# Performance work log

Measured on AMD Instinct MI355X. Metric: run time of the kernel, lower is better.

## Reference

```python
import jax, jax.numpy as jnp
import numpy as np

TWO_PI = 2.0 * np.pi
PI = np.pi
RESONANCE_WEIGHT = 0.1


def setup_inputs() -> dict:
    key = jax.random.key(0)
    k1, k2, k3, k4, k5 = jax.random.split(key, 5)
    B, C = 16384, 1000          # batch, num classes for the CE term
    N, E = 4096, 131072         # graph nodes, directed edges (avg degree 32)
    outputs = jax.random.normal(k1, (B, C), dtype=jnp.float32)
    targets = jax.random.randint(k2, (B,), 0, C)
    resonance_phase = jax.random.normal(k3, (N, N), dtype=jnp.float32)
    edge_src = jax.random.randint(k4, (E,), 0, N)
    edge_dst = jax.random.randint(k5, (E,), 0, N)
    return {"outputs": outputs, "targets": targets,
            "resonance_phase": resonance_phase,
            "edge_src": edge_src, "edge_dst": edge_dst}


def reference(outputs, targets, resonance_phase, edge_src, edge_dst):
    # base_criterion: CrossEntropyLoss (mean reduction over batch)
    logp = jax.nn.log_softmax(outputs, axis=-1)                      # [B, C]
    base_loss = -jnp.mean(jnp.take_along_axis(logp, targets[:, None], axis=1))

    # resonance term: vectorized gather over all topology edges
    phase_ij = resonance_phase[edge_src, edge_dst]                   # [E]
    phase_ji = resonance_phase[edge_dst, edge_src]                   # [E]
    d = jnp.abs(phase_ij - phase_ji) % TWO_PI
    d = jnp.where(d > PI, TWO_PI - d, d)                             # wrap to [0, pi]
    resonance_loss = jnp.sum(d) / d.shape[0]                         # / total_connections

    return base_loss + RESONANCE_WEIGHT * resonance_loss
```

## Files before the change

kernel.cpp:

```cpp
#include <hip/hip_runtime.h>
#include <math.h>

#define TWO_PI_F 6.28318530717958647692f
#define PI_F     3.14159265358979323846f

__global__ __launch_bounds__(256) void fused_kernel(
    const float* __restrict__ outputs,
    const int*   __restrict__ targets,
    const float* __restrict__ phase,
    const int*   __restrict__ esrc,
    const int*   __restrict__ edst,
    int B, int C, int N, int E,
    int res_blocks,
    float invB, float scaleE,
    float* __restrict__ ws)
{
    __shared__ float part[4];
    const int lane = threadIdx.x & 63;
    const int wave = threadIdx.x >> 6;

    float wsum = 0.0f;

    if ((int)blockIdx.x < res_blocks) {
        const int i = blockIdx.x * blockDim.x + threadIdx.x;
        float d = 0.0f;
        if (i < E) {
            const int s = esrc[i];
            const int t = edst[i];
            const float a = phase[(size_t)s * (size_t)N + (size_t)t];
            const float b = phase[(size_t)t * (size_t)N + (size_t)s];
            d = fabsf(a - b);
            d = fmodf(d, TWO_PI_F);
            if (d > PI_F) d = TWO_PI_F - d;
        }
        #pragma unroll
        for (int off = 32; off; off >>= 1)
            d += __shfl_xor(d, off, 64);
        if (lane == 0) wsum = d * scaleE;
    } else {
        const int row = (blockIdx.x - res_blocks) * 4 + wave;
        if (row < B) {
            const float*  rowp = outputs + (size_t)row * (size_t)C;
            const float4* row4 = (const float4*)rowp;
            const int nf4 = C >> 2;

            float m, s;
            if (nf4 <= 256) {
                const float4 NEG = make_float4(-INFINITY, -INFINITY, -INFINITY, -INFINITY);
                const int j0 = lane, j1 = lane + 64, j2 = lane + 128, j3 = lane + 192;
                float4 v0 = (j0 < nf4) ? row4[j0] : NEG;
                float4 v1 = (j1 < nf4) ? row4[j1] : NEG;
                float4 v2 = (j2 < nf4) ? row4[j2] : NEG;
                float4 v3 = (j3 < nf4) ? row4[j3] : NEG;
                const int remBase = nf4 << 2;
                const bool hasTail = (remBase + lane) < C;
                float tail = hasTail ? rowp[remBase + lane] : -INFINITY;

                m = tail;
                m = fmaxf(m, fmaxf(fmaxf(v0.x, v0.y), fmaxf(v0.z, v0.w)));
                m = fmaxf(m, fmaxf(fmaxf(v1.x, v1.y), fmaxf(v1.z, v1.w)));
                m = fmaxf(m, fmaxf(fmaxf(v2.x, v2.y), fmaxf(v2.z, v2.w)));
                m = fmaxf(m, fmaxf(fmaxf(v3.x, v3.y), fmaxf(v3.z, v3.w)));
                #pragma unroll
                for (int off = 32; off; off >>= 1)
                    m = fmaxf(m, __shfl_xor(m, off, 64));

                s  = __expf(v0.x - m) + __expf(v0.y - m) + __expf(v0.z - m) + __expf(v0.w - m);
                s += __expf(v1.x - m) + __expf(v1.y - m) + __expf(v1.z - m) + __expf(v1.w - m);
                s += __expf(v2.x - m) + __expf(v2.y - m) + __expf(v2.z - m) + __expf(v2.w - m);
                s += __expf(v3.x - m) + __expf(v3.y - m) + __expf(v3.z - m) + __expf(v3.w - m);
                s += __expf(tail - m);
                #pragma unroll
                for (int off = 32; off; off >>= 1)
                    s += __shfl_xor(s, off, 64);
            } else {
                m = -INFINITY;
                for (int j = lane; j < nf4; j += 64) {
                    float4 x = row4[j];
                    m = fmaxf(m, fmaxf(fmaxf(x.x, x.y), fmaxf(x.z, x.w)));
                }
                const int remBase = nf4 << 2;
                if (remBase + lane < C) m = fmaxf(m, rowp[remBase + lane]);
                #pragma unroll
                for (int off = 32; off; off >>= 1)
                    m = fmaxf(m, __shfl_xor(m, off, 64));

                s = 0.0f;
                for (int j = lane; j < nf4; j += 64) {
                    float4 x = row4[j];
                    s += __expf(x.x - m) + __expf(x.y - m)
                       + __expf(x.z - m) + __expf(x.w - m);
                }
                if (remBase + lane < C) s += __expf(rowp[remBase + lane] - m);
                #pragma unroll
                for (int off = 32; off; off >>= 1)
                    s += __shfl_xor(s, off, 64);
            }

            if (lane == 0) {
                const int t = targets[row];
                const float tv = rowp[t];
                wsum = (m + __logf(s) - tv) * invB;
            }
        }
    }

    if (lane == 0) part[wave] = wsum;
    __syncthreads();
    if (threadIdx.x == 0)
        ws[blockIdx.x] = part[0] + part[1] + part[2] + part[3];
}

__global__ __launch_bounds__(256) void reduce_kernel(
    const float* __restrict__ ws, int P, float* __restrict__ out)
{
    float s = 0.0f;
    for (int i = threadIdx.x; i < P; i += 256)
        s += ws[i];
    #pragma unroll
    for (int off = 32; off; off >>= 1)
        s += __shfl_xor(s, off, 64);

    __shared__ float part[4];
    if ((threadIdx.x & 63) == 0) part[threadIdx.x >> 6] = s;
    __syncthreads();
    if (threadIdx.x == 0)
        out[0] = part[0] + part[1] + part[2] + part[3];
}

extern "C" void kernel_launch(void* const* d_in, const int* in_sizes, int n_in,
                              void* d_out, int out_size, void* d_ws, size_t ws_size,
                              hipStream_t stream) {
    const float* outputs = (const float*)d_in[0];
    const int*   targets = (const int*)d_in[1];
    const float* phase   = (const float*)d_in[2];
    const int*   esrc    = (const int*)d_in[3];
    const int*   edst    = (const int*)d_in[4];

    const int B = in_sizes[1];
    const int C = in_sizes[0] / B;
    const int E = in_sizes[3];
    int N = 1;
    while ((long long)N * (long long)N < (long long)in_sizes[2]) N++;

    const int res_blocks = (E + 255) / 256;
    const int ce_blocks  = (B + 3) / 4;
    const int grid = res_blocks + ce_blocks;

    float* ws = (float*)d_ws;

    fused_kernel<<<grid, 256, 0, stream>>>(outputs, targets, phase, esrc, edst,
                                           B, C, N, E, res_blocks,
                                           1.0f / (float)B, 0.1f / (float)E,
                                           ws);
    reduce_kernel<<<1, 256, 0, stream>>>(ws, grid, (float*)d_out);
}
```

Baseline: 148.4 us.

## Process four edges per thread and two CE rows per wave

The resonance branch now has each thread load four edges through int4 index loads and issue eight independent phase gathers, which cuts the resonance block count by four. The cross-entropy branch has each wave handle two rows in sequence, halving the CE block count, and the target value load is moved earlier. The aim is to raise memory-level parallelism per thread and reduce block launch and partial-sum overhead, at the cost of more registers and fewer total waves to hide latency. Helper functions factor out the warp reductions and the shared per-row CE code.

Result: no change. 149.7 us (+0.9%).

```diff
diff --git a/kernel.cpp b/kernel.cpp
--- a/kernel.cpp
+++ b/kernel.cpp
@@ -3,6 +3,72 @@
 
 #define TWO_PI_F 6.28318530717958647692f
 #define PI_F     3.14159265358979323846f
+
+__device__ __forceinline__ float warp_sum(float s) {
+    #pragma unroll
+    for (int off = 32; off; off >>= 1) s += __shfl_xor(s, off, 64);
+    return s;
+}
+__device__ __forceinline__ float warp_max(float m) {
+    #pragma unroll
+    for (int off = 32; off; off >>= 1) m = fmaxf(m, __shfl_xor(m, off, 64));
+    return m;
+}
+
+__device__ __forceinline__ float edge_wrap(float a, float b) {
+    float d = fabsf(a - b);
+    d = fmodf(d, TWO_PI_F);
+    return (d > PI_F) ? (TWO_PI_F - d) : d;
+}
+
+__device__ __forceinline__ float ce_row(const float* __restrict__ rowp,
+                                        int C, int lane, int t) {
+    const float4* row4 = (const float4*)rowp;
+    const int nf4 = C >> 2;
+    const float tv = rowp[t];
+    float m, s;
+    if (nf4 <= 256) {
+        const float4 NEG = make_float4(-INFINITY, -INFINITY, -INFINITY, -INFINITY);
+        const int j0 = lane, j1 = lane + 64, j2 = lane + 128, j3 = lane + 192;
+        float4 v0 = (j0 < nf4) ? row4[j0] : NEG;
+        float4 v1 = (j1 < nf4) ? row4[j1] : NEG;
+        float4 v2 = (j2 < nf4) ? row4[j2] : NEG;
+        float4 v3 = (j3 < nf4) ? row4[j3] : NEG;
+        const int remBase = nf4 << 2;
+        float tail = (remBase + lane < C) ? rowp[remBase + lane] : -INFINITY;
+
+        m = tail;
+        m = fmaxf(m, fmaxf(fmaxf(v0.x, v0.y), fmaxf(v0.z, v0.w)));
+        m = fmaxf(m, fmaxf(fmaxf(v1.x, v1.y), fmaxf(v1.z, v1.w)));
+        m = fmaxf(m, fmaxf(fmaxf(v2.x, v2.y), fmaxf(v2.z, v2.w)));
+        m = fmaxf(m, fmaxf(fmaxf(v3.x, v3.y), fmaxf(v3.z, v3.w)));
+        m = warp_max(m);
+
+        s  = __expf(v0.x - m) + __expf(v0.y - m) + __expf(v0.z - m) + __expf(v0.w - m);
+        s += __expf(v1.x - m) + __expf(v1.y - m) + __expf(v1.z - m) + __expf(v1.w - m);
+        s += __expf(v2.x - m) + __expf(v2.y - m) + __expf(v2.z - m) + __expf(v2.w - m);
+        s += __expf(v3.x - m) + __expf(v3.y - m) + __expf(v3.z - m) + __expf(v3.w - m);
+        s += __expf(tail - m);
+        s = warp_sum(s);
+    } else {
+        m = -INFINITY;
+        for (int j = lane; j < nf4; j += 64) {
+            float4 x = row4[j];
+            m = fmaxf(m, fmaxf(fmaxf(x.x, x.y), fmaxf(x.z, x.w)));
+        }
+        const int remBase = nf4 << 2;
+        if (remBase + lane < C) m = fmaxf(m, rowp[remBase + lane]);
+        m = warp_max(m);
+        s = 0.0f;
+        for (int j = lane; j < nf4; j += 64) {
+            float4 x = row4[j];
+            s += __expf(x.x - m) + __expf(x.y - m) + __expf(x.z - m) + __expf(x.w - m);
+        }
+        if (remBase + lane < C) s += __expf(rowp[remBase + lane] - m);
+        s = warp_sum(s);
+    }
+    return m + __logf(s) - tv;
+}
 
 __global__ __launch_bounds__(256) void fused_kernel(
     const float* __restrict__ outputs,
@@ -22,86 +88,41 @@
     float wsum = 0.0f;
 
     if ((int)blockIdx.x < res_blocks) {
-        const int i = blockIdx.x * blockDim.x + threadIdx.x;
+        const int base = (blockIdx.x * 256 + threadIdx.x) * 4;
         float d = 0.0f;
-        if (i < E) {
-            const int s = esrc[i];
-            const int t = edst[i];
-            const float a = phase[(size_t)s * (size_t)N + (size_t)t];
-            const float b = phase[(size_t)t * (size_t)N + (size_t)s];
-            d = fabsf(a - b);
-            d = fmodf(d, TWO_PI_F);
-            if (d > PI_F) d = TWO_PI_F - d;
+        if (base + 3 < E) {
+            const int4 s4 = *(const int4*)(esrc + base);
+            const int4 t4 = *(const int4*)(edst + base);
+            const float a0 = phase[(size_t)s4.x * (size_t)N + (size_t)t4.x];
+            const float b0 = phase[(size_t)t4.x * (size_t)N + (size_t)s4.x];
+            const float a1 = phase[(size_t)s4.y * (size_t)N + (size_t)t4.y];
+            const float b1 = phase[(size_t)t4.y * (size_t)N + (size_t)s4.y];
+            const float a2 = phase[(size_t)s4.z * (size_t)N + (size_t)t4.z];
+            const float b2 = phase[(size_t)t4.z * (size_t)N + (size_t)s4.z];
+            const float a3 = phase[(size_t)s4.w * (size_t)N + (size_t)t4.w];
+            const float b3 = phase[(size_t)t4.w * (size_t)N + (size_t)s4.w];
+            d = edge_wrap(a0, b0) + edge_wrap(a1, b1)
+              + edge_wrap(a2, b2) + edge_wrap(a3, b3);
+        } else {
+            for (int i = base; i < E; i++) {
+                const int s = esrc[i], t = edst[i];
+                d += edge_wrap(phase[(size_t)s * (size_t)N + (size_t)t],
+                               phase[(size_t)t * (size_t)N + (size_t)s]);
+            }
         }
-        #pragma unroll
-        for (int off = 32; off; off >>= 1)
-            d += __shfl_xor(d, off, 64);
+        d = warp_sum(d);
         if (lane == 0) wsum = d * scaleE;
     } else {
-        const int row = (blockIdx.x - res_blocks) * 4 + wave;
-        if (row < B) {
-            const float*  rowp = outputs + (size_t)row * (size_t)C;
-            const float4* row4 = (const float4*)rowp;
-            const int nf4 = C >> 2;
-
-            float m, s;
-            if (nf4 <= 256) {
-                const float4 NEG = make_float4(-INFINITY, -INFINITY, -INFINITY, -INFINITY);
-                const int j0 = lane, j1 = lane + 64, j2 = lane + 128, j3 = lane + 192;
-                float4 v0 = (j0 < nf4) ? row4[j0] : NEG;
-                float4 v1 = (j1 < nf4) ? row4[j1] : NEG;
-                float4 v2 = (j2 < nf4) ? row4[j2] : NEG;
-                float4 v3 = (j3 < nf4) ? row4[j3] : NEG;
-                const int remBase = nf4 << 2;
-                const bool hasTail = (remBase + lane) < C;
-                float tail = hasTail ? rowp[remBase + lane] : -INFINITY;
-
-                m = tail;
-                m = fmaxf(m, fmaxf(fmaxf(v0.x, v0.y), fmaxf(v0.z, v0.w)));
-                m = fmaxf(m, fmaxf(fmaxf(v1.x, v1.y), fmaxf(v1.z, v1.w)));
-                m = fmaxf(m, fmaxf(fmaxf(v2.x, v2.y), fmaxf(v2.z, v2.w)));
-                m = fmaxf(m, fmaxf(fmaxf(v3.x, v3.y), fmaxf(v3.z, v3.w)));
-                #pragma unroll
-                for (int off = 32; off; off >>= 1)
-                    m = fmaxf(m, __shfl_xor(m, off, 64));
-
-                s  = __expf(v0.x - m) + __expf(v0.y - m) + __expf(v0.z - m) + __expf(v0.w - m);
-                s += __expf(v1.x - m) + __expf(v1.y - m) + __expf(v1.z - m) + __expf(v1.w - m);
-                s += __expf(v2.x - m) + __expf(v2.y - m) + __expf(v2.z - m) + __expf(v2.w - m);
-                s += __expf(v3.x - m) + __expf(v3.y - m) + __expf(v3.z - m) + __expf(v3.w - m);
-                s += __expf(tail - m);
-                #pragma unroll
-                for (int off = 32; off; off >>= 1)
-                    s += __shfl_xor(s, off, 64);
-            } else {
-                m = -INFINITY;
-                for (int j = lane; j < nf4; j += 64) {
-                    float4 x = row4[j];
-                    m = fmaxf(m, fmaxf(fmaxf(x.x, x.y), fmaxf(x.z, x.w)));
-                }
-                const int remBase = nf4 << 2;
-                if (remBase + lane < C) m = fmaxf(m, rowp[remBase + lane]);
-                #pragma unroll
-                for (int off = 32; off; off >>= 1)
-                    m = fmaxf(m, __shfl_xor(m, off, 64));
-
-                s = 0.0f;
-                for (int j = lane; j < nf4; j += 64) {
-                    float4 x = row4[j];
-                    s += __expf(x.x - m) + __expf(x.y - m)
-                       + __expf(x.z - m) + __expf(x.w - m);
-                }
-                if (remBase + lane < C) s += __expf(rowp[remBase + lane] - m);
-                #pragma unroll
-                for (int off = 32; off; off >>= 1)
-                    s += __shfl_xor(s, off, 64);
-            }
-
-            if (lane == 0) {
-                const int t = targets[row];
-                const float tv = rowp[t];
-                wsum = (m + __logf(s) - tv) * invB;
-            }
+        const int row0 = ((int)blockIdx.x - res_blocks) * 8 + wave * 2;
+        if (row0 < B) {
+            const int t0 = targets[row0];
+            const float c0 = ce_row(outputs + (size_t)row0 * (size_t)C, C, lane, t0);
+            if (lane == 0) wsum += c0 * invB;
+        }
+        if (row0 + 1 < B) {
+            const int t1 = targets[row0 + 1];
+            const float c1 = ce_row(outputs + (size_t)(row0 + 1) * (size_t)C, C, lane, t1);
+            if (lane == 0) wsum += c1 * invB;
         }
     }
 
@@ -117,10 +138,7 @@
     float s = 0.0f;
     for (int i = threadIdx.x; i < P; i += 256)
         s += ws[i];
-    #pragma unroll
-    for (int off = 32; off; off >>= 1)
-        s += __shfl_xor(s, off, 64);
-
+    s = warp_sum(s);
     __shared__ float part[4];
     if ((threadIdx.x & 63) == 0) part[threadIdx.x >> 6] = s;
     __syncthreads();
@@ -143,8 +161,8 @@
     int N = 1;
     while ((long long)N * (long long)N < (long long)in_sizes[2]) N++;
 
-    const int res_blocks = (E + 255) / 256;
-    const int ce_blocks  = (B + 3) / 4;
+    const int res_blocks = (E + 1023) / 1024;
+    const int ce_blocks  = (B + 7) / 8;
     const int grid = res_blocks + ce_blocks;
 
     float* ws = (float*)d_ws;
```
